# Kernel tuning notes

Measured on AMD Instinct MI355X. Metric: run time of the kernel, lower is better.

The kernel has to match this reference:

```python
import jax, jax.numpy as jnp
import numpy as np

IN_CH, OUT_CH, L, INTERVAL = 128, 128, 80, 5
NCPT = int(np.ceil(L / INTERVAL)) + 1            # 17 anchor points
INTERVAL2 = 1 if INTERVAL == 1 else L - (NCPT - 2) * INTERVAL  # 5
P = (L + 1) ** 2                                  # 6561 positions
# static repeat_interleave index: degree l occupies 2l+1 positions
REPEAT_IDX = np.repeat(np.arange(L + 1), 2 * np.arange(L + 1) + 1)  # [P]


def setup_inputs() -> dict:
    key = jax.random.key(0)
    kx, kw = jax.random.split(key)
    x = jax.random.normal(kx, (16, IN_CH, P), dtype=jnp.float32)
    stdv = 1.0 / float(np.sqrt(IN_CH * (L + 1)))
    weight = jax.random.uniform(kw, (IN_CH, OUT_CH, NCPT, 1), dtype=jnp.float32,
                                minval=-stdv, maxval=stdv)
    return {"x": x, "weight": weight}


def _interp_filter(weight):
    # weight: [in, out, ncpt, 1] -> per-degree coeffs [in, out, L+1]
    w = weight[..., 0]                                   # [in, out, ncpt]
    l0 = jnp.arange(INTERVAL, dtype=w.dtype) / INTERVAL  # [interval]
    # segments between anchors 0..ncpt-2: [in, out, ncpt-2, interval]
    w1 = (1.0 - l0) * w[:, :, :-2, None] + l0 * w[:, :, 1:-1, None]
    w1 = w1.reshape(w.shape[0], w.shape[1], -1)          # [in, out, (ncpt-2)*interval]
    l1 = jnp.arange(INTERVAL2 + 1, dtype=w.dtype) / INTERVAL2  # [interval2+1]
    w2 = (1.0 - l1) * w[:, :, -2, None] + l1 * w[:, :, -1, None]  # [in, out, interval2+1]
    wl = jnp.concatenate([w1, w2], axis=2)               # [in, out, L+1]
    return wl[:, :, REPEAT_IDX]                          # [in, out, P]


def reference(x, weight):
    wp = _interp_filter(weight)                          # [in, out, P]
    # out[b,o,p] = sum_i wp[i,o,p] * x[b,i,p]  (fused, no [b,in,out,P] temp)
    return jnp.einsum('iop,bip->bop', wp, x)
```

## Files before the change

### kernel.cpp

```cpp
#include <hip/hip_runtime.h>

#define IC    128
#define OC    128
#define NL    81
#define PTOT  6561
#define NCPT  17
#define BSTR  (IC*PTOT)
#define NBLK  1568

typedef short short8 __attribute__((ext_vector_type(8)));
typedef float f32x4  __attribute__((ext_vector_type(4)));

__device__ __forceinline__ unsigned short f2bf(float x) {
    unsigned u = __float_as_uint(x);
    return (unsigned short)((u + 0x7FFFu + ((u >> 16) & 1u)) >> 16);
}

__global__ __launch_bounds__(256) void shconv_prep(const float* __restrict__ w,
                                                   unsigned short* __restrict__ WtF) {
    const int l    = blockIdx.x >> 2;
    const int quad = blockIdx.x & 3;
    int s; float fr;
    if (l < 75) { s = l / 5;  fr = (float)(l - s * 5) * 0.2f; }
    else        { s = 15;     fr = (float)(l - 75) * 0.2f;    }
    unsigned short* dst = WtF + (size_t)l * (OC * IC);
    const int e0 = quad * 4096;
    for (int e = e0 + threadIdx.x; e < e0 + 4096; e += 256) {
        int j  = e & 7;
        int mm = (e >> 3) & 15;
        int gg = (e >> 7) & 3;
        int kk = (e >> 9) & 3;
        int of = e >> 11;
        int o = of * 16 + mm;
        int i = kk * 32 + gg * 8 + j;
        const float* wp = w + i * (OC * NCPT) + o * NCPT + s;
        float v = (1.0f - fr) * wp[0] + fr * wp[1];
        dst[e] = f2bf(v);
    }
}

__global__ __launch_bounds__(256, 2) void shconv_main(const float* __restrict__ x,
                                                      const unsigned short* __restrict__ WtF,
                                                      float* __restrict__ out) {
    const int bid = blockIdx.x;
    const int b   = bid / 98;
    const int r   = bid - b * 98;
    int l, chunk;
    if (r < 64) { l = r; chunk = 0; }
    else        { int rr = r - 64; l = 64 + (rr >> 1); chunk = rr & 1; }

    const int p2     = l * l;
    const int len    = 2 * l + 1;
    const int pstart = p2 & ~3;

    const int tid  = threadIdx.x;
    const int wave = tid >> 6;
    const int lane = tid & 63;
    const int m    = lane & 15;
    const int g    = lane >> 4;
    const int nh   = wave & 1;
    const int mh   = wave >> 1;

    const int pcol = pstart + chunk * 128 + nh * 64 + 4 * m;
    int pr = pcol; if (pr > PTOT - 4) pr = PTOT - 4;

    const float* xg = x + (size_t)b * BSTR + (size_t)(g * 8) * PTOT + pr;
    const unsigned short* wf = WtF + (size_t)l * (OC * IC) + (size_t)mh * 8192
                                   + (size_t)lane * 8;

    f32x4 acc[4][4];
    #pragma unroll
    for (int of = 0; of < 4; ++of)
        #pragma unroll
        for (int d = 0; d < 4; ++d) acc[of][d] = (f32x4){0.f, 0.f, 0.f, 0.f};

    #pragma unroll
    for (int kk = 0; kk < 4; ++kk) {
        float v[8][4];
        #pragma unroll
        for (int j = 0; j < 8; ++j)
            #pragma unroll
            for (int d = 0; d < 4; ++d)
                v[j][d] = xg[(size_t)(kk * 32 + j) * PTOT + d];

        short8 bfr[4];
        #pragma unroll
        for (int d = 0; d < 4; ++d)
            #pragma unroll
            for (int j = 0; j < 8; ++j)
                bfr[d][j] = (short)f2bf(v[j][d]);

        short8 af[4];
        #pragma unroll
        for (int of = 0; of < 4; ++of)
            af[of] = *(const short8*)(wf + ((size_t)(of * 4 + kk) << 9));

        #pragma unroll
        for (int of = 0; of < 4; ++of)
            #pragma unroll
            for (int d = 0; d < 4; ++d)
                acc[of][d] = __builtin_amdgcn_mfma_f32_16x16x32_bf16(af[of], bfr[d], acc[of][d], 0, 0, 0);
    }

    float* ob0 = out + (size_t)b * (OC * PTOT);
    const int phi = p2 + len;
    #pragma unroll
    for (int of = 0; of < 4; ++of) {
        const int obase = (mh * 4 + of) * 16 + g * 4;
        #pragma unroll
        for (int j = 0; j < 4; ++j) {
            float* ob = ob0 + (size_t)(obase + j) * PTOT;
            #pragma unroll
            for (int d = 0; d < 4; ++d) {
                int p = pr + d;
                if (p >= p2 && p < phi) ob[p] = acc[of][d][j];
            }
        }
    }
}

extern "C" void kernel_launch(void* const* d_in, const int* in_sizes, int n_in,
                              void* d_out, int out_size, void* d_ws, size_t ws_size,
                              hipStream_t stream) {
    const float* x = (const float*)d_in[0];
    const float* w = (const float*)d_in[1];
    unsigned short* WtF = (unsigned short*)d_ws;
    float* out = (float*)d_out;

    shconv_prep<<<dim3(NL * 4), dim3(256), 0, stream>>>(w, WtF);
    shconv_main<<<dim3(NBLK),   dim3(256), 0, stream>>>(x, WtF, out);
}
```

Baseline: 139.8 us.

## Stage x tiles in LDS via direct global-to-LDS loads with smaller per-block chunks

```diff
diff --git a/kernel.cpp b/kernel.cpp
--- a/kernel.cpp
+++ b/kernel.cpp
@@ -1,4 +1,5 @@
 #include <hip/hip_runtime.h>
+#include <stdint.h>
 
 #define IC    128
 #define OC    128
@@ -6,10 +7,18 @@
 #define PTOT  6561
 #define NCPT  17
 #define BSTR  (IC*PTOT)
-#define NBLK  1568
+#define XN    (16*BSTR)
+#define NPB   147
+#define NBLK  (16*NPB)
+
+#define ROWF  72
+#define ROWB  (ROWF*4)
 
 typedef short short8 __attribute__((ext_vector_type(8)));
 typedef float f32x4  __attribute__((ext_vector_type(4)));
+
+#define AS1 __attribute__((address_space(1)))
+#define AS3 __attribute__((address_space(3)))
 
 __device__ __forceinline__ unsigned short f2bf(float x) {
     unsigned u = __float_as_uint(x);
@@ -39,81 +48,98 @@
     }
 }
 
-__global__ __launch_bounds__(256, 2) void shconv_main(const float* __restrict__ x,
+__global__ __launch_bounds__(256, 4) void shconv_main(const float* __restrict__ x,
                                                       const unsigned short* __restrict__ WtF,
                                                       float* __restrict__ out) {
+    __shared__ float sx[128 * ROWF];
+
     const int bid = blockIdx.x;
-    const int b   = bid / 98;
-    const int r   = bid - b * 98;
+    const int b   = bid / NPB;
+    const int r0  = bid - b * NPB;
     int l, chunk;
-    if (r < 64) { l = r; chunk = 0; }
-    else        { int rr = r - 64; l = 64 + (rr >> 1); chunk = rr & 1; }
+    if (r0 < 32)      { l = r0;               chunk = 0; }
+    else if (r0 < 96) { int rr = r0 - 32; l = 32 + (rr >> 1); chunk = rr & 1; }
+    else              { int rr = r0 - 96; int q3 = rr / 3; l = 64 + q3; chunk = rr - q3 * 3; }
 
-    const int p2     = l * l;
-    const int len    = 2 * l + 1;
-    const int pstart = p2 & ~3;
+    const int plen = 2 * l + 1;
+    const int pw   = l * l + chunk * 64;
+    int lenw = plen - chunk * 64; if (lenw > 64) lenw = 64;
 
     const int tid  = threadIdx.x;
-    const int wave = tid >> 6;
+    const int wq   = tid >> 6;
     const int lane = tid & 63;
-    const int m    = lane & 15;
-    const int g    = lane >> 4;
-    const int nh   = wave & 1;
-    const int mh   = wave >> 1;
 
-    const int pcol = pstart + chunk * 128 + nh * 64 + 4 * m;
-    int pr = pcol; if (pr > PTOT - 4) pr = PTOT - 4;
+    #pragma unroll
+    for (int i = 0; i < 9; ++i) {
+        const int ldsoff = wq * 9216 + i * 1024;
+        int off = ldsoff + lane * 16;
+        int r   = (unsigned)off / ROWB;
+        int c   = off - r * ROWB;
+        int ch  = ((r & 15) << 3) | (r >> 4);
+        int R   = ch * PTOT + pw;
+        int A4  = R & ~3;
+        int s   = R - A4;
+        int needC = (4 * (s + lenw) - 1) & ~15;
+        int ce  = c < needC ? c : needC;
+        long fidx = (long)b * BSTR + A4 + (ce >> 2);
+        if (fidx > (long)XN - 4) fidx = (long)XN - 4;
+        __builtin_amdgcn_global_load_lds((const AS1 uint32_t*)(x + fidx),
+                                         (AS3 uint32_t*)(sx + (ldsoff >> 2)),
+                                         16, 0, 0);
+    }
+    asm volatile("s_waitcnt vmcnt(0)" ::: "memory");
+    __syncthreads();
 
-    const float* xg = x + (size_t)b * BSTR + (size_t)(g * 8) * PTOT + pr;
-    const unsigned short* wf = WtF + (size_t)l * (OC * IC) + (size_t)mh * 8192
-                                   + (size_t)lane * 8;
+    const int m  = lane & 15;
+    const int g  = lane >> 4;
+    const int mh = wq >> 1;
+    const int nh = wq & 1;
 
-    f32x4 acc[4][4];
+    const unsigned short* wfb = WtF + (size_t)l * (OC * IC) + (size_t)mh * 8192
+                                    + (size_t)lane * 8;
+
+    f32x4 acc[4][2];
     #pragma unroll
     for (int of = 0; of < 4; ++of)
         #pragma unroll
-        for (int d = 0; d < 4; ++d) acc[of][d] = (f32x4){0.f, 0.f, 0.f, 0.f};
+        for (int pt = 0; pt < 2; ++pt) acc[of][pt] = (f32x4){0.f, 0.f, 0.f, 0.f};
 
     #pragma unroll
     for (int kk = 0; kk < 4; ++kk) {
-        float v[8][4];
-        #pragma unroll
-        for (int j = 0; j < 8; ++j)
-            #pragma unroll
-            for (int d = 0; d < 4; ++d)
-                v[j][d] = xg[(size_t)(kk * 32 + j) * PTOT + d];
-
-        short8 bfr[4];
-        #pragma unroll
-        for (int d = 0; d < 4; ++d)
-            #pragma unroll
-            for (int j = 0; j < 8; ++j)
-                bfr[d][j] = (short)f2bf(v[j][d]);
-
-        short8 af[4];
+        short8 wfr[4];
         #pragma unroll
         for (int of = 0; of < 4; ++of)
-            af[of] = *(const short8*)(wf + ((size_t)(of * 4 + kk) << 9));
+            wfr[of] = *(const short8*)(wfb + ((size_t)(of * 4 + kk) << 9));
 
         #pragma unroll
-        for (int of = 0; of < 4; ++of)
+        for (int pt = 0; pt < 2; ++pt) {
+            const int pl = nh * 32 + pt * 16 + m;
+            short8 bfr;
             #pragma unroll
-            for (int d = 0; d < 4; ++d)
-                acc[of][d] = __builtin_amdgcn_mfma_f32_16x16x32_bf16(af[of], bfr[d], acc[of][d], 0, 0, 0);
+            for (int j = 0; j < 8; ++j) {
+                int ch  = kk * 32 + g * 8 + j;
+                int row = ((ch & 7) << 4) | (ch >> 3);
+                int sc  = (ch + pw) & 3;
+                bfr[j] = (short)f2bf(sx[row * ROWF + sc + pl]);
+            }
+            #pragma unroll
+            for (int of = 0; of < 4; ++of)
+                acc[of][pt] = __builtin_amdgcn_mfma_f32_16x16x32_bf16(wfr[of], bfr, acc[of][pt], 0, 0, 0);
+        }
     }
 
     float* ob0 = out + (size_t)b * (OC * PTOT);
-    const int phi = p2 + len;
     #pragma unroll
     for (int of = 0; of < 4; ++of) {
-        const int obase = (mh * 4 + of) * 16 + g * 4;
         #pragma unroll
-        for (int j = 0; j < 4; ++j) {
-            float* ob = ob0 + (size_t)(obase + j) * PTOT;
-            #pragma unroll
-            for (int d = 0; d < 4; ++d) {
-                int p = pr + d;
-                if (p >= p2 && p < phi) ob[p] = acc[of][d][j];
+        for (int pt = 0; pt < 2; ++pt) {
+            const int pl = nh * 32 + pt * 16 + m;
+            const int pd = chunk * 64 + pl;
+            if (pd < plen) {
+                const int p = l * l + pd;
+                #pragma unroll
+                for (int j = 0; j < 4; ++j)
+                    ob0[(size_t)(mh * 64 + of * 16 + g * 4 + j) * PTOT + p] = acc[of][pt][j];
             }
         }
     }
```

After: 127.0 us. 1.1x faster.

## Stage x tiles into LDS via async global_load_lds, double-buffered across two batches

Applied to the files above, without the earlier changes.

```diff
diff --git a/kernel.cpp b/kernel.cpp
--- a/kernel.cpp
+++ b/kernel.cpp
@@ -1,4 +1,5 @@
 #include <hip/hip_runtime.h>
+#include <stdint.h>
 
 #define IC    128
 #define OC    128
@@ -6,10 +7,19 @@
 #define PTOT  6561
 #define NCPT  17
 #define BSTR  (IC*PTOT)
-#define NBLK  1568
+#define XN    (16*BSTR)
+#define NLC   147
+#define NBLK  1176
+
+#define ROWF  72
+#define ROWB  (ROWF*4)
+#define BUFF  (128*ROWF)
 
 typedef short short8 __attribute__((ext_vector_type(8)));
 typedef float f32x4  __attribute__((ext_vector_type(4)));
+
+#define AS1 __attribute__((address_space(1)))
+#define AS3 __attribute__((address_space(3)))
 
 __device__ __forceinline__ unsigned short f2bf(float x) {
     unsigned u = __float_as_uint(x);
@@ -42,81 +52,130 @@
 __global__ __launch_bounds__(256, 2) void shconv_main(const float* __restrict__ x,
                                                       const unsigned short* __restrict__ WtF,
                                                       float* __restrict__ out) {
-    const int bid = blockIdx.x;
-    const int b   = bid / 98;
-    const int r   = bid - b * 98;
+    __shared__ float sx[2 * BUFF];
+
+    const int k  = blockIdx.x;
+    const int lc = k >> 3;
+    const int b0 = (k & 7) << 1;
     int l, chunk;
-    if (r < 64) { l = r; chunk = 0; }
-    else        { int rr = r - 64; l = 64 + (rr >> 1); chunk = rr & 1; }
+    if (lc < 32)      { l = lc;                    chunk = 0; }
+    else if (lc < 96) { int rr = lc - 32; l = 32 + (rr >> 1); chunk = rr & 1; }
+    else              { int rr = lc - 96; int q3 = rr / 3; l = 64 + q3; chunk = rr - q3 * 3; }
 
-    const int p2     = l * l;
-    const int len    = 2 * l + 1;
-    const int pstart = p2 & ~3;
+    const int plen = 2 * l + 1;
+    const int pw   = l * l + chunk * 64;
+    int lenw = plen - chunk * 64; if (lenw > 64) lenw = 64;
 
     const int tid  = threadIdx.x;
-    const int wave = tid >> 6;
+    const int wq   = tid >> 6;
     const int lane = tid & 63;
     const int m    = lane & 15;
     const int g    = lane >> 4;
-    const int nh   = wave & 1;
-    const int mh   = wave >> 1;
+    const int mh   = wq >> 1;
+    const int nh   = wq & 1;
 
-    const int pcol = pstart + chunk * 128 + nh * 64 + 4 * m;
-    int pr = pcol; if (pr > PTOT - 4) pr = PTOT - 4;
+    const unsigned short* wfb = WtF + (size_t)l * (OC * IC) + (size_t)mh * 8192
+                                    + (size_t)lane * 8;
+    short8 wfr[16];
+    #pragma unroll
+    for (int f = 0; f < 16; ++f)
+        wfr[f] = *(const short8*)(wfb + ((size_t)f << 9));
+    __builtin_amdgcn_sched_barrier(0);
 
-    const float* xg = x + (size_t)b * BSTR + (size_t)(g * 8) * PTOT + pr;
-    const unsigned short* wf = WtF + (size_t)l * (OC * IC) + (size_t)mh * 8192
-                                   + (size_t)lane * 8;
+#define STAGE(BUF, BB)                                                          \
+    {                                                                           \
+        _Pragma("unroll")                                                       \
+        for (int i = 0; i < 9; ++i) {                                           \
+            const int ldsoff = wq * 9216 + i * 1024;                            \
+            int off = ldsoff + lane * 16;                                       \
+            int r   = (unsigned)off / ROWB;                                     \
+            int c   = off - r * ROWB;                                           \
+            int ch  = ((r & 15) << 3) | (r >> 4);                               \
+            int R   = ch * PTOT + pw;                                           \
+            int A4  = R & ~3;                                                   \
+            int s   = R - A4;                                                   \
+            int needC = (4 * (s + lenw) - 1) & ~15;                             \
+            int ce  = c < needC ? c : needC;                                    \
+            long fidx = (long)(BB) * BSTR + A4 + (ce >> 2);                     \
+            if (fidx > (long)XN - 4) fidx = (long)XN - 4;                       \
+            __builtin_amdgcn_global_load_lds((const AS1 uint32_t*)(x + fidx),   \
+                (AS3 uint32_t*)(sx + (BUF) * BUFF + (ldsoff >> 2)), 16, 0, 0);  \
+        }                                                                       \
+    }
 
-    f32x4 acc[4][4];
+#define MFMA_PHASE(BUF, ACC)                                                    \
+    {                                                                           \
+        _Pragma("unroll")                                                       \
+        for (int kk = 0; kk < 4; ++kk) {                                        \
+            _Pragma("unroll")                                                   \
+            for (int pt = 0; pt < 2; ++pt) {                                    \
+                const int pl = nh * 32 + pt * 16 + m;                           \
+                short8 bfr;                                                     \
+                _Pragma("unroll")                                               \
+                for (int j = 0; j < 8; ++j) {                                   \
+                    int ch  = kk * 32 + g * 8 + j;                              \
+                    int row = ((ch & 7) << 4) | (ch >> 3);                      \
+                    int sc  = (ch + pw) & 3;                                    \
+                    bfr[j] = (short)f2bf(sx[(BUF) * BUFF + row * ROWF + sc + pl]); \
+                }                                                               \
+                _Pragma("unroll")                                               \
+                for (int of = 0; of < 4; ++of)                                  \
+                    ACC[of][pt] = __builtin_amdgcn_mfma_f32_16x16x32_bf16(      \
+                        wfr[of * 4 + kk], bfr, ACC[of][pt], 0, 0, 0);           \
+            }                                                                   \
+        }                                                                       \
+    }
+
+#define STORES(ACC, BB)                                                         \
+    {                                                                           \
+        float* ob0 = out + (size_t)(BB) * (OC * PTOT);                          \
+        _Pragma("unroll")                                                       \
+        for (int of = 0; of < 4; ++of) {                                        \
+            _Pragma("unroll")                                                   \
+            for (int pt = 0; pt < 2; ++pt) {                                    \
+                const int pl = nh * 32 + pt * 16 + m;                           \
+                const int pd = chunk * 64 + pl;                                 \
+                if (pd < plen) {                                                \
+                    const int p = l * l + pd;                                   \
+                    _Pragma("unroll")                                           \
+                    for (int j = 0; j < 4; ++j)                                 \
+                        ob0[(size_t)(mh * 64 + of * 16 + g * 4 + j) * PTOT + p] \
+                            = ACC[of][pt][j];                                   \
+                }                                                               \
+            }                                                                   \
+        }                                                                       \
+    }
+
+    STAGE(0, b0)
+    asm volatile("s_waitcnt vmcnt(0)" ::: "memory");
+    __builtin_amdgcn_sched_barrier(0);
+    __builtin_amdgcn_s_barrier();
+
+    STAGE(1, b0 + 1)
+    f32x4 acc0[4][2];
     #pragma unroll
     for (int of = 0; of < 4; ++of)
         #pragma unroll
-        for (int d = 0; d < 4; ++d) acc[of][d] = (f32x4){0.f, 0.f, 0.f, 0.f};
+        for (int pt = 0; pt < 2; ++pt) acc0[of][pt] = (f32x4){0.f, 0.f, 0.f, 0.f};
+    MFMA_PHASE(0, acc0)
 
+    asm volatile("s_waitcnt vmcnt(0)" ::: "memory");
+    __builtin_amdgcn_sched_barrier(0);
+    __builtin_amdgcn_s_barrier();
+
+    STORES(acc0, b0)
+
+    f32x4 acc1[4][2];
     #pragma unroll
-    for (int kk = 0; kk < 4; ++kk) {
-        float v[8][4];
+    for (int of = 0; of < 4; ++of)
         #pragma unroll
-        for (int j = 0; j < 8; ++j)
-            #pragma unroll
-            for (int d = 0; d < 4; ++d)
-                v[j][d] = xg[(size_t)(kk * 32 + j) * PTOT + d];
+        for (int pt = 0; pt < 2; ++pt) acc1[of][pt] = (f32x4){0.f, 0.f, 0.f, 0.f};
+    MFMA_PHASE(1, acc1)
+    STORES(acc1, b0 + 1)
 
-        short8 bfr[4];
-        #pragma unroll
-        for (int d = 0; d < 4; ++d)
-            #pragma unroll
-            for (int j = 0; j < 8; ++j)
-                bfr[d][j] = (short)f2bf(v[j][d]);
-
-        short8 af[4];
-        #pragma unroll
-        for (int of = 0; of < 4; ++of)
-            af[of] = *(const short8*)(wf + ((size_t)(of * 4 + kk) << 9));
-
-        #pragma unroll
-        for (int of = 0; of < 4; ++of)
-            #pragma unroll
-            for (int d = 0; d < 4; ++d)
-                acc[of][d] = __builtin_amdgcn_mfma_f32_16x16x32_bf16(af[of], bfr[d], acc[of][d], 0, 0, 0);
-    }
-
-    float* ob0 = out + (size_t)b * (OC * PTOT);
-    const int phi = p2 + len;
-    #pragma unroll
-    for (int of = 0; of < 4; ++of) {
-        const int obase = (mh * 4 + of) * 16 + g * 4;
-        #pragma unroll
-        for (int j = 0; j < 4; ++j) {
-            float* ob = ob0 + (size_t)(obase + j) * PTOT;
-            #pragma unroll
-            for (int d = 0; d < 4; ++d) {
-                int p = pr + d;
-                if (p >= p2 && p < phi) ob[p] = acc[of][d][j];
-            }
-        }
-    }
+#undef STAGE
+#undef MFMA_PHASE
+#undef STORES
 }
 
 extern "C" void kernel_launch(void* const* d_in, const int* in_sizes, int n_in,
```

New measurement: 126.2 us. 9.7% less time.
